# Performance work log

Measured on AMD Instinct MI355X. Metric: run time of the kernel, lower is better.

## Reference

```python
import jax, jax.numpy as jnp
import numpy as np

SIGMA = 2.0
RADIUS = 2.5


def setup_inputs() -> dict:
    key = jax.random.key(0)
    k0, k1, k2, k3, k4, k5 = jax.random.split(key, 6)
    Nq, Ns, K, Kp, Cin, Cout = 50000, 50000, 32, 15, 64, 64
    s_feats = jax.random.uniform(k0, (Ns, Cin), dtype=jnp.float32)
    q_points = jax.random.normal(k1, (Nq, 3), dtype=jnp.float32)
    s_points = jax.random.normal(k2, (Ns, 3), dtype=jnp.float32)
    neighbor_indices = jax.random.randint(k3, (Nq, K), 0, Ns)
    # rigid kernel point dispositions within the kernel radius (load_kernels stand-in)
    kernel_points = jax.random.uniform(k4, (Kp, 3), minval=-1.0, maxval=1.0,
                                       dtype=jnp.float32) * (RADIUS * 0.66)
    # kaiming_uniform_ with a=sqrt(5) -> bound = 1/sqrt(fan_in)
    bound = 1.0 / np.sqrt(Cin)
    weights = jax.random.uniform(k5, (Kp, Cin, Cout), minval=-bound, maxval=bound,
                                 dtype=jnp.float32)
    return dict(s_feats=s_feats, q_points=q_points, s_points=s_points,
                neighbor_indices=neighbor_indices, kernel_points=kernel_points,
                weights=weights)


def reference(s_feats, q_points, s_points, neighbor_indices, kernel_points, weights):
    # pad support points with a far-away shadow point (index Ns)
    shadow_pt = jnp.full((1, s_points.shape[1]), 1e6, dtype=s_points.dtype)
    s_pts = jnp.concatenate([s_points, shadow_pt], axis=0)
    # gather neighbor coordinates, center on query points: [Nq, K, 3]
    neighbors = s_pts[neighbor_indices] - q_points[:, None, :]
    # squared distance to each kernel point: [Nq, K, Kp]
    sq_distances = jnp.sum((neighbors[:, :, None, :] - kernel_points[None, None]) ** 2,
                           axis=-1)
    # linear correlation influence, clamped at 0: [Nq, K, Kp]
    all_weights = jnp.maximum(1.0 - jnp.sqrt(sq_distances) / SIGMA, 0.0)
    # pad support features with a zero shadow feature row
    sf = jnp.concatenate([s_feats, jnp.zeros((1, s_feats.shape[1]), s_feats.dtype)],
                         axis=0)
    neighb_x = sf[neighbor_indices]  # [Nq, K, Cin]
    # aggregate neighbor features per kernel point: [Nq, Kp, Cin]
    weighted = jnp.einsum('nkp,nkc->npc', all_weights, neighb_x)
    # apply per-kernel-point weight matrices and sum over kernel points: [Nq, Cout]
    output_features = jnp.einsum('npc,pcd->nd', weighted, weights)
    # density normalization: count valid (non-shadow, positive-sum) neighbors
    neighbor_features_sum = jnp.sum(neighb_x, axis=-1)          # [Nq, K]
    neighbor_num = jnp.sum(neighbor_features_sum > 0.0, axis=-1)  # [Nq]
    neighbor_num = jnp.maximum(neighbor_num, 1)
    return output_features / neighbor_num[:, None].astype(output_features.dtype)
```

## Files before the change

kernel.cpp:

```cpp
#include <hip/hip_runtime.h>
#include <hip/hip_bf16.h>

typedef __attribute__((ext_vector_type(8))) short short8;
typedef __attribute__((ext_vector_type(4))) float f32x4;

#define WT_BYTE_OFF 6400000

#define QSTRIDE   2064
#define XSLICE    4128
#define LDS_NN    33024
#define LDS_POS   33088
#define POSSTRIDE 768
#define LDS_RED   33088
#define LDS_TOT   (33088 + 8*768)

__device__ inline unsigned short f2bf(float x) {
    unsigned int u = __float_as_uint(x);
    unsigned int r = (u + 0x7FFFu + ((u >> 16) & 1u)) >> 16;
    return (unsigned short)r;
}

__device__ inline unsigned short f2bf_fast(float x) {
    __hip_bfloat16 b = __float2bfloat16(x);
    return *reinterpret_cast<unsigned short*>(&b);
}

__global__ void kpconv_pre(const float* __restrict__ s_feats,
                           const float* __restrict__ weights,
                           unsigned short* __restrict__ xbf,
                           unsigned short* __restrict__ wfrag) {
    int t = blockIdx.x * 256 + threadIdx.x;
    if (t < 800000) {
        int i = t * 4;
        float4 v = *(const float4*)(s_feats + i);
        ushort4 o;
        o.x = f2bf(v.x); o.y = f2bf(v.y); o.z = f2bf(v.z); o.w = f2bf(v.w);
        *(ushort4*)(xbf + i) = o;
    } else {
        int tw = t - 800000;
        if (tw < 8192) {
            const int f = tw >> 6, l = tw & 63;
            const int m = l & 15, h = l >> 4;
            const int dt = f >> 5, kh = (f >> 4) & 1, jj = f & 15;
            const int d = dt * 16 + m;
            const int pcb = (kh * 16 + jj) * 32 + 8 * h;
            ushort4 o0, o1;
            unsigned short* op0 = (unsigned short*)&o0;
            unsigned short* op1 = (unsigned short*)&o1;
            #pragma unroll
            for (int e = 0; e < 8; ++e) {
                const int pc = pcb + e;
                const int p = pc & 15, c = pc >> 4;
                const float wv = (p < 15) ? weights[(p * 64 + c) * 64 + d] : 0.0f;
                if (e < 4) op0[e] = f2bf(wv); else op1[e - 4] = f2bf(wv);
            }
            *(ushort4*)(wfrag + tw * 8) = o0;
            *(ushort4*)(wfrag + tw * 8 + 4) = o1;
        }
    }
}

__global__ __launch_bounds__(512, 8) void kpconv_main(
    const float* __restrict__ qpts, const float* __restrict__ spts,
    const int* __restrict__ nbr, const float* __restrict__ kpts,
    const unsigned short* __restrict__ xbf, const unsigned short* __restrict__ wfrag,
    float* __restrict__ out)
{
    __shared__ __attribute__((aligned(128))) unsigned char lds[LDS_TOT];
    const int tid = threadIdx.x;
    const int w = tid >> 6;
    const int l = tid & 63;
    const int h = l >> 4;
    const int m = l & 15;
    const int qbase = blockIdx.x * 16;

    const int pm = (m < 15) ? m : 14;
    const float kx = kpts[pm * 3 + 0], ky = kpts[pm * 3 + 1], kz = kpts[pm * 3 + 2];

    unsigned char* xw = lds + w * XSLICE;
    unsigned char* posb = lds + LDS_POS + w * POSSTRIDE;

    const int* nbase = nbr + (qbase + 2 * w) * 32;
    const int sBoth = nbase[l];

    const int voff = l >> 3;
    int sidx[2][4];
    #pragma unroll
    for (int i = 0; i < 2; ++i)
        #pragma unroll
        for (int g = 0; g < 4; ++g)
            sidx[i][g] = nbase[32 * i + 8 * g + voff];

    const float2 pxy = *(const float2*)(spts + (size_t)sBoth * 3);
    const float pz = spts[(size_t)sBoth * 3 + 2];

    int4 xv[2][4];
    #pragma unroll
    for (int i = 0; i < 2; ++i)
        #pragma unroll
        for (int g = 0; g < 4; ++g)
            xv[i][g] = *(const int4*)(xbf + (size_t)sidx[i][g] * 64 + (l & 7) * 8);

    *(float2*)(posb + l * 8) = pxy;
    *(float*)(posb + 512 + l * 4) = pz;

    const int eb = (l >> 2) & 1;
    unsigned char* wb2base = xw + (l & 7) * 512 + (l >> 3) * 2;
    unsigned char* wb2E = wb2base + eb * 64;
    unsigned char* wb2O = wb2base + (eb ^ 1) * 64;
    const int xb2 = (l & 3) << 4;
    unsigned char* rb3a = xw + m * 64;
    unsigned char* rb3b = xw + (m ^ 1) * 64;
    const int rxb = (h ^ (m >> 3)) << 4;

    uint2 pk0[4];

    #pragma unroll
    for (int i = 0; i < 2; ++i) {
        const int ql = 2 * w + i;
        const int q = qbase + ql;

        int nn = 0;
        #pragma unroll
        for (int g = 0; g < 4; ++g) {
            const int4 v = xv[i][g];
            unsigned long long b = __ballot((v.x | v.y | v.z | v.w) != 0);
            b |= b >> 4; b |= b >> 2; b |= b >> 1;
            nn += __popcll(b & 0x0101010101010101ULL);
        }
        if (nn < 1) nn = 1;
        if (l == 0) *(int*)(lds + LDS_NN + ql * 4) = nn;

        #pragma unroll
        for (int g = 0; g < 4; ++g) {
            const unsigned short* u8 = (const unsigned short*)&xv[i][g];
            const int gofs = (g << 4) ^ xb2;
            unsigned char* wgE = wb2E + gofs;
            unsigned char* wgO = wb2O + gofs;
            #pragma unroll
            for (int t = 0; t < 4; ++t) {
                *(unsigned short*)(wgE + t * 128) = u8[2 * t];
                *(unsigned short*)(wgO + t * 128) = u8[2 * t + 1];
            }
        }

        const float qx = qpts[q * 3 + 0], qy = qpts[q * 3 + 1], qz = qpts[q * 3 + 2];
        const float bx = qx + kx, by = qy + ky, bz = qz + kz;
        float wv[8];
        #pragma unroll
        for (int j = 0; j < 8; ++j) {
            const float2 sxy = *(const float2*)(posb + (32 * i + j) * 8 + h * 64);
            const float sz = *(const float*)(posb + 512 + (32 * i + j) * 4 + h * 32);
            const float dx = sxy.x - bx, dy = sxy.y - by, dz = sz - bz;
            const float d2 = __builtin_fmaf(dx, dx,
                             __builtin_fmaf(dy, dy, dz * dz));
            const float s = __builtin_amdgcn_sqrtf(d2);
            wv[j] = fmaxf(__builtin_fmaf(s, -0.5f, 1.0f), 0.0f);
        }
        union { unsigned int d[4]; short8 s8; } au;
        const bool pad = (m == 15);
        #pragma unroll
        for (int jp = 0; jp < 4; ++jp) {
            const unsigned int pk = (unsigned int)f2bf_fast(wv[2 * jp]) |
                                    ((unsigned int)f2bf_fast(wv[2 * jp + 1]) << 16);
            au.d[jp] = pad ? 0u : pk;
        }

        f32x4 c3[4];
        #pragma unroll
        for (int ct = 0; ct < 4; ++ct) {
            const unsigned char* rb = (ct < 2) ? rb3a : rb3b;
            short8 b3 = *(const short8*)(rb + ct * 1024 + (rxb ^ ((ct & 1) << 5)));
            f32x4 z = {0.f, 0.f, 0.f, 0.f};
            c3[ct] = __builtin_amdgcn_mfma_f32_16x16x32_bf16(au.s8, b3, z, 0, 0, 0);
        }

        #pragma unroll
        for (int ct = 0; ct < 4; ++ct) {
            uint2 pkv;
            pkv.x = (unsigned int)f2bf_fast(c3[ct][0]) | ((unsigned int)f2bf_fast(c3[ct][1]) << 16);
            pkv.y = (unsigned int)f2bf_fast(c3[ct][2]) | ((unsigned int)f2bf_fast(c3[ct][3]) << 16);
            if (i == 0) {
                pk0[ct] = pkv;
            } else {
                *(uint2*)(lds + ql * QSTRIDE + (ct * 16 + m) * 32 + h * 8) = pkv;
            }
        }
    }

    #pragma unroll
    for (int ct = 0; ct < 4; ++ct)
        *(uint2*)(lds + (2 * w) * QSTRIDE + (ct * 16 + m) * 32 + h * 8) = pk0[ct];

    __syncthreads();

    const int dt = w & 3, kh = w >> 2;
    const int d = dt * 16 + m;
    f32x4 acc0 = {0.f, 0.f, 0.f, 0.f}, acc1 = {0.f, 0.f, 0.f, 0.f};
    const unsigned char* abase = lds + m * QSTRIDE + 16 * h;
    const unsigned short* bbase = wfrag + (size_t)((dt * 2 + kh) * 16) * 512 + l * 8;
    const int k0 = kh * 16;
    #pragma unroll
    for (int j = 0; j < 8; ++j) {
        short8 a4a = *(const short8*)(abase + (k0 + j) * 64);
        short8 b4a = *(const short8*)(bbase + j * 512);
        acc0 = __builtin_amdgcn_mfma_f32_16x16x32_bf16(a4a, b4a, acc0, 0, 0, 0);
        short8 a4b = *(const short8*)(abase + (k0 + 8 + j) * 64);
        short8 b4b = *(const short8*)(bbase + (8 + j) * 512);
        acc1 = __builtin_amdgcn_mfma_f32_16x16x32_bf16(a4b, b4b, acc1, 0, 0, 0);
    }

    if (kh == 1) {
        f32x4 acc = acc0 + acc1;
        *(f32x4*)(lds + LDS_RED + dt * 1024 + l * 16) = acc;
    }
    __syncthreads();
    if (kh == 0) {
        f32x4 part = *(const f32x4*)(lds + LDS_RED + dt * 1024 + l * 16);
        #pragma unroll
        for (int r = 0; r < 4; ++r) {
            const int qr = 4 * h + r;
            const int nn = *(const int*)(lds + LDS_NN + qr * 4);
            out[(size_t)(qbase + qr) * 64 + d] =
                (acc0[r] + acc1[r] + part[r]) * (1.0f / (float)nn);
        }
    }
}

extern "C" void kernel_launch(void* const* d_in, const int* in_sizes, int n_in,
                              void* d_out, int out_size, void* d_ws, size_t ws_size,
                              hipStream_t stream) {
    const float* s_feats = (const float*)d_in[0];
    const float* q_points = (const float*)d_in[1];
    const float* s_points = (const float*)d_in[2];
    const int* nbr = (const int*)d_in[3];
    const float* kpts = (const float*)d_in[4];
    const float* wts = (const float*)d_in[5];
    float* out = (float*)d_out;

    unsigned short* xbf = (unsigned short*)d_ws;
    unsigned short* wfrag = (unsigned short*)((char*)d_ws + WT_BYTE_OFF);

    hipLaunchKernelGGL(kpconv_pre, dim3(3157), dim3(256), 0, stream,
                       s_feats, wts, xbf, wfrag);
    hipLaunchKernelGGL(kpconv_main, dim3(3125), dim3(512), 0, stream,
                       q_points, s_points, nbr, kpts, xbf, wfrag, out);
}
```

Baseline: 52.35 us.

## Pad support points to float4, share neighbor indices via bpermute, vectorize LDS reads

The pre-pass now also writes support points padded to float4, so the main kernel fetches each neighbor position with one 16-byte gather instead of a float2 plus a float load. Neighbor indices for the feature gathers come from ds_bpermute on the already-loaded index register rather than eight extra global loads. The distance loop reads two positions per LDS access with wider vector loads. In exchange the pre-pass grows by 50k threads and writes an extra 800KB buffer that the main kernel must read back.

```diff
diff --git a/kernel.cpp b/kernel.cpp
--- a/kernel.cpp
+++ b/kernel.cpp
@@ -4,7 +4,8 @@
 typedef __attribute__((ext_vector_type(8))) short short8;
 typedef __attribute__((ext_vector_type(4))) float f32x4;
 
-#define WT_BYTE_OFF 6400000
+#define WT_BYTE_OFF  6400000
+#define SP4_BYTE_OFF 6531072
 
 #define QSTRIDE   2064
 #define XSLICE    4128
@@ -27,8 +28,10 @@
 
 __global__ void kpconv_pre(const float* __restrict__ s_feats,
                            const float* __restrict__ weights,
+                           const float* __restrict__ spts,
                            unsigned short* __restrict__ xbf,
-                           unsigned short* __restrict__ wfrag) {
+                           unsigned short* __restrict__ wfrag,
+                           float* __restrict__ spts4) {
     int t = blockIdx.x * 256 + threadIdx.x;
     if (t < 800000) {
         int i = t * 4;
@@ -56,12 +59,22 @@
             }
             *(ushort4*)(wfrag + tw * 8) = o0;
             *(ushort4*)(wfrag + tw * 8 + 4) = o1;
+        } else {
+            int ts = tw - 8192;
+            if (ts < 50000) {
+                float4 o;
+                o.x = spts[ts * 3 + 0];
+                o.y = spts[ts * 3 + 1];
+                o.z = spts[ts * 3 + 2];
+                o.w = 0.0f;
+                *(float4*)(spts4 + ts * 4) = o;
+            }
         }
     }
 }
 
 __global__ __launch_bounds__(512, 8) void kpconv_main(
-    const float* __restrict__ qpts, const float* __restrict__ spts,
+    const float* __restrict__ qpts, const float* __restrict__ spts4,
     const int* __restrict__ nbr, const float* __restrict__ kpts,
     const unsigned short* __restrict__ xbf, const unsigned short* __restrict__ wfrag,
     float* __restrict__ out)
@@ -83,16 +96,16 @@
     const int* nbase = nbr + (qbase + 2 * w) * 32;
     const int sBoth = nbase[l];
 
-    const int voff = l >> 3;
+    const int voff4 = (l >> 3) << 2;
     int sidx[2][4];
     #pragma unroll
     for (int i = 0; i < 2; ++i)
         #pragma unroll
         for (int g = 0; g < 4; ++g)
-            sidx[i][g] = nbase[32 * i + 8 * g + voff];
-
-    const float2 pxy = *(const float2*)(spts + (size_t)sBoth * 3);
-    const float pz = spts[(size_t)sBoth * 3 + 2];
+            sidx[i][g] = __builtin_amdgcn_ds_bpermute(
+                             voff4 + ((32 * i + 8 * g) << 2), sBoth);
+
+    const f32x4 pv4 = *(const f32x4*)(spts4 + (size_t)sBoth * 4);
 
     int4 xv[2][4];
     #pragma unroll
@@ -101,8 +114,9 @@
         for (int g = 0; g < 4; ++g)
             xv[i][g] = *(const int4*)(xbf + (size_t)sidx[i][g] * 64 + (l & 7) * 8);
 
+    float2 pxy; pxy.x = pv4[0]; pxy.y = pv4[1];
     *(float2*)(posb + l * 8) = pxy;
-    *(float*)(posb + 512 + l * 4) = pz;
+    *(float*)(posb + 512 + l * 4) = pv4[2];
 
     const int eb = (l >> 2) & 1;
     unsigned char* wb2base = xw + (l & 7) * 512 + (l >> 3) * 2;
@@ -148,14 +162,19 @@
         const float bx = qx + kx, by = qy + ky, bz = qz + kz;
         float wv[8];
         #pragma unroll
-        for (int j = 0; j < 8; ++j) {
-            const float2 sxy = *(const float2*)(posb + (32 * i + j) * 8 + h * 64);
-            const float sz = *(const float*)(posb + 512 + (32 * i + j) * 4 + h * 32);
-            const float dx = sxy.x - bx, dy = sxy.y - by, dz = sz - bz;
-            const float d2 = __builtin_fmaf(dx, dx,
-                             __builtin_fmaf(dy, dy, dz * dz));
-            const float s = __builtin_amdgcn_sqrtf(d2);
-            wv[j] = fmaxf(__builtin_fmaf(s, -0.5f, 1.0f), 0.0f);
+        for (int jp = 0; jp < 4; ++jp) {
+            const f32x4 xy2 = *(const f32x4*)(posb + (32 * i + 2 * jp) * 8 + h * 64);
+            const float2 z2 = *(const float2*)(posb + 512 + (32 * i + 2 * jp) * 4 + h * 32);
+            const float dx0 = xy2[0] - bx, dy0 = xy2[1] - by, dz0 = z2.x - bz;
+            const float d20 = __builtin_fmaf(dx0, dx0,
+                              __builtin_fmaf(dy0, dy0, dz0 * dz0));
+            wv[2 * jp] = fmaxf(__builtin_fmaf(
+                             __builtin_amdgcn_sqrtf(d20), -0.5f, 1.0f), 0.0f);
+            const float dx1 = xy2[2] - bx, dy1 = xy2[3] - by, dz1 = z2.y - bz;
+            const float d21 = __builtin_fmaf(dx1, dx1,
+                              __builtin_fmaf(dy1, dy1, dz1 * dz1));
+            wv[2 * jp + 1] = fmaxf(__builtin_fmaf(
+                             __builtin_amdgcn_sqrtf(d21), -0.5f, 1.0f), 0.0f);
         }
         union { unsigned int d[4]; short8 s8; } au;
         const bool pad = (m == 15);
@@ -240,9 +259,10 @@
 
     unsigned short* xbf = (unsigned short*)d_ws;
     unsigned short* wfrag = (unsigned short*)((char*)d_ws + WT_BYTE_OFF);
-
-    hipLaunchKernelGGL(kpconv_pre, dim3(3157), dim3(256), 0, stream,
-                       s_feats, wts, xbf, wfrag);
+    float* spts4 = (float*)((char*)d_ws + SP4_BYTE_OFF);
+
+    hipLaunchKernelGGL(kpconv_pre, dim3(3353), dim3(256), 0, stream,
+                       s_feats, wts, s_points, xbf, wfrag, spts4);
     hipLaunchKernelGGL(kpconv_main, dim3(3125), dim3(512), 0, stream,
-                       q_points, s_points, nbr, kpts, xbf, wfrag, out);
-}
+                       q_points, spts4, nbr, kpts, xbf, wfrag, out);
+}
```

Result: no change. 52.93 us (+1.1%).

## Halve query tile to 8 per block and drop cross-wave K-split reduction

Applied to the files above, without the earlier changes.

Each block now handles 8 queries with 4 waves instead of 16 queries with 8 waves. Each wave computes one 16-column output tile over the full 32-step K loop, which removes the LDS partial-sum reduction and the second barrier. LDS use per block roughly halves, so more blocks can be resident. In exchange, half the MFMA rows are wasted: rows 8-15 duplicate queries 0-7 and are discarded. Weight fragments are also reloaded twice as often across the grid.

```diff
diff --git a/kernel.cpp b/kernel.cpp
--- a/kernel.cpp
+++ b/kernel.cpp
@@ -8,11 +8,10 @@
 
 #define QSTRIDE   2064
 #define XSLICE    4128
-#define LDS_NN    33024
-#define LDS_POS   33088
+#define LDS_NN    16512
+#define LDS_POS   16544
 #define POSSTRIDE 768
-#define LDS_RED   33088
-#define LDS_TOT   (33088 + 8*768)
+#define LDS_TOT   (16544 + 4*768)
 
 __device__ inline unsigned short f2bf(float x) {
     unsigned int u = __float_as_uint(x);
@@ -60,7 +59,7 @@
     }
 }
 
-__global__ __launch_bounds__(512, 8) void kpconv_main(
+__global__ __launch_bounds__(256, 8) void kpconv_main(
     const float* __restrict__ qpts, const float* __restrict__ spts,
     const int* __restrict__ nbr, const float* __restrict__ kpts,
     const unsigned short* __restrict__ xbf, const unsigned short* __restrict__ wfrag,
@@ -72,7 +71,7 @@
     const int l = tid & 63;
     const int h = l >> 4;
     const int m = l & 15;
-    const int qbase = blockIdx.x * 16;
+    const int qbase = blockIdx.x * 8;
 
     const int pm = (m < 15) ? m : 14;
     const float kx = kpts[pm * 3 + 0], ky = kpts[pm * 3 + 1], kz = kpts[pm * 3 + 2];
@@ -194,35 +193,25 @@
 
     __syncthreads();
 
-    const int dt = w & 3, kh = w >> 2;
-    const int d = dt * 16 + m;
-    f32x4 acc0 = {0.f, 0.f, 0.f, 0.f}, acc1 = {0.f, 0.f, 0.f, 0.f};
-    const unsigned char* abase = lds + m * QSTRIDE + 16 * h;
-    const unsigned short* bbase = wfrag + (size_t)((dt * 2 + kh) * 16) * 512 + l * 8;
-    const int k0 = kh * 16;
-    #pragma unroll
-    for (int j = 0; j < 8; ++j) {
-        short8 a4a = *(const short8*)(abase + (k0 + j) * 64);
-        short8 b4a = *(const short8*)(bbase + j * 512);
-        acc0 = __builtin_amdgcn_mfma_f32_16x16x32_bf16(a4a, b4a, acc0, 0, 0, 0);
-        short8 a4b = *(const short8*)(abase + (k0 + 8 + j) * 64);
-        short8 b4b = *(const short8*)(bbase + (8 + j) * 512);
-        acc1 = __builtin_amdgcn_mfma_f32_16x16x32_bf16(a4b, b4b, acc1, 0, 0, 0);
-    }
-
-    if (kh == 1) {
-        f32x4 acc = acc0 + acc1;
-        *(f32x4*)(lds + LDS_RED + dt * 1024 + l * 16) = acc;
-    }
-    __syncthreads();
-    if (kh == 0) {
-        f32x4 part = *(const f32x4*)(lds + LDS_RED + dt * 1024 + l * 16);
+    const int dt = w;
+    const int m2 = m & 7;
+    f32x4 acc = {0.f, 0.f, 0.f, 0.f};
+    const unsigned char* abase = lds + m2 * QSTRIDE + 16 * h;
+    const unsigned short* bbase = wfrag + (size_t)(dt * 32) * 512 + l * 8;
+    #pragma unroll
+    for (int j = 0; j < 32; ++j) {
+        short8 a4 = *(const short8*)(abase + j * 64);
+        short8 b4 = *(const short8*)(bbase + j * 512);
+        acc = __builtin_amdgcn_mfma_f32_16x16x32_bf16(a4, b4, acc, 0, 0, 0);
+    }
+
+    if (h < 2) {
         #pragma unroll
         for (int r = 0; r < 4; ++r) {
             const int qr = 4 * h + r;
             const int nn = *(const int*)(lds + LDS_NN + qr * 4);
-            out[(size_t)(qbase + qr) * 64 + d] =
-                (acc0[r] + acc1[r] + part[r]) * (1.0f / (float)nn);
+            out[(size_t)(qbase + qr) * 64 + dt * 16 + m] =
+                acc[r] * (1.0f / (float)nn);
         }
     }
 }
@@ -243,6 +232,6 @@
 
     hipLaunchKernelGGL(kpconv_pre, dim3(3157), dim3(256), 0, stream,
                        s_feats, wts, xbf, wfrag);
-    hipLaunchKernelGGL(kpconv_main, dim3(3125), dim3(512), 0, stream,
+    hipLaunchKernelGGL(kpconv_main, dim3(6250), dim3(256), 0, stream,
                        q_points, s_points, nbr, kpts, xbf, wfrag, out);
 }
```

New measurement: 63.88 us. 22.0% more time.
